# Kernel optimization log

Measured on AMD Instinct MI355X. Metric: run time of the kernel, lower is better.

The kernel has to match this reference:

```python
import jax, jax.numpy as jnp
import numpy as np

B, S, E, H = 2, 2048, 2048, 16
NOPE, ROPE, VD = 128, 64, 128
QH = NOPE + ROPE  # 192
LORA = 512
ROPE_THETA = 10000.0
EPS = 1e-6


def setup_inputs() -> dict:
    key = jax.random.key(0)
    ks = jax.random.split(key, 5)
    sd = lambda n: 1.0 / np.sqrt(n)
    return {
        "x": jax.random.normal(ks[0], (B, S, E), jnp.float32),
        "wq": jax.random.normal(ks[1], (E, H * QH), jnp.float32) * sd(E),
        "wkv_a": jax.random.normal(ks[2], (E, LORA + ROPE), jnp.float32) * sd(E),
        "wkv_b": jax.random.normal(ks[3], (LORA, H * (NOPE + VD)), jnp.float32) * sd(LORA),
        "wo": jax.random.normal(ks[4], (H * VD, E), jnp.float32) * sd(H * VD),
        "kv_norm_scale": jnp.ones((LORA,), jnp.float32),
    }


def _rope(xp, cos, sin):
    # xp: (..., s, d); cos/sin: (s, d//2)
    d2 = xp.shape[-1] // 2
    x1, x2 = xp[..., :d2], xp[..., d2:]
    return jnp.concatenate([x1 * cos - x2 * sin, x2 * cos + x1 * sin], axis=-1)


def reference(x, wq, wkv_a, wkv_b, wo, kv_norm_scale):
    b, s, _ = x.shape
    # queries: (b, H, s, QH), split into no-pe / pe slices
    q = (x @ wq).reshape(b, s, H, QH).transpose(0, 2, 1, 3)
    q_nope, q_pe = q[..., :NOPE], q[..., NOPE:]

    # low-rank KV latent projection
    kva = x @ wkv_a  # (b, s, LORA + ROPE)
    ckv, k_pe = kva[..., :LORA], kva[..., LORA:]
    ckv = ckv * jax.lax.rsqrt(jnp.mean(ckv * ckv, axis=-1, keepdims=True) + EPS)
    ckv = ckv * kv_norm_scale  # RMSNorm on latent
    kv = (ckv @ wkv_b).reshape(b, s, H, NOPE + VD).transpose(0, 2, 1, 3)
    k_nope, v = kv[..., :NOPE], kv[..., NOPE:]

    # partial RoPE on the rope slice only
    pos = jnp.arange(s, dtype=jnp.float32)
    inv = 1.0 / (ROPE_THETA ** (jnp.arange(0, ROPE, 2, dtype=jnp.float32) / ROPE))
    ang = pos[:, None] * inv  # (s, ROPE//2)
    cos, sin = jnp.cos(ang), jnp.sin(ang)
    q_pe = _rope(q_pe, cos, sin)                 # (b, H, s, ROPE)
    k_pe = _rope(k_pe[:, None, :, :], cos, sin)  # (b, 1, s, ROPE), shared over heads

    # concat (the new_empty + slice-write in torch)
    qs = jnp.concatenate([q_nope, q_pe], axis=-1)  # (b, H, s, QH)
    ks_ = jnp.concatenate(
        [k_nope, jnp.broadcast_to(k_pe, (b, H, s, ROPE))], axis=-1
    )  # (b, H, s, QH)

    # causal SDPA with scale = q_head_dim**-0.5; asymmetric V head dim
    scale = QH ** -0.5
    scores = jnp.einsum('bhqd,bhkd->bhqk', qs, ks_) * scale
    causal = jnp.tril(jnp.ones((s, s), dtype=bool))
    scores = jnp.where(causal, scores, jnp.finfo(scores.dtype).min)
    attn = jax.nn.softmax(scores, axis=-1)
    out = jnp.einsum('bhqk,bhkd->bhqd', attn, v)  # (b, H, s, VD)
    out = out.transpose(0, 2, 1, 3).reshape(b, s, H * VD)
    return out @ wo
```

## Files before the change

kernel.cpp:

```cpp
#include <hip/hip_runtime.h>
#include <stdint.h>
#include <stddef.h>

typedef __bf16 bf16x8 __attribute__((ext_vector_type(8)));
typedef float floatx4 __attribute__((ext_vector_type(4)));
typedef unsigned short u16;

__device__ __forceinline__ float bf2f(u16 h) {
    unsigned u = ((unsigned)h) << 16;
    return __builtin_bit_cast(float, u);
}
__device__ __forceinline__ u16 f2bf(float f) {
    unsigned u = __builtin_bit_cast(unsigned, f);
    u += 0x7fffu + ((u >> 16) & 1u);
    return (u16)(u >> 16);
}

__device__ __forceinline__ void gload16(const void* g, void* l) {
    __builtin_amdgcn_global_load_lds(
        (const __attribute__((address_space(1))) uint32_t*)g,
        (__attribute__((address_space(3))) uint32_t*)l, 16, 0, 0);
}

__device__ __forceinline__ void wait_vm8() { asm volatile("s_waitcnt vmcnt(8)" ::: "memory"); }
__device__ __forceinline__ void wait_vm6() { asm volatile("s_waitcnt vmcnt(6)" ::: "memory"); }
__device__ __forceinline__ void wait_vm4() { asm volatile("s_waitcnt vmcnt(4)" ::: "memory"); }
__device__ __forceinline__ void wait_vm3() { asm volatile("s_waitcnt vmcnt(3)" ::: "memory"); }
__device__ __forceinline__ void wait_vm0() { asm volatile("s_waitcnt vmcnt(0)" ::: "memory"); }

__global__ __launch_bounds__(256) void k_conv_x(const float* __restrict__ in,
                                                u16* __restrict__ out, int n8) {
    int i = blockIdx.x * 256 + threadIdx.x;
    if (i >= n8) return;
    const float* f = in + (size_t)i * 8;
    unsigned o[4];
    for (int t = 0; t < 4; t++) {
        u16 lo = f2bf(f[2 * t]), hi = f2bf(f[2 * t + 1]);
        o[t] = (unsigned)lo | ((unsigned)hi << 16);
    }
    uint4 p = {o[0], o[1], o[2], o[3]};
    *(uint4*)&out[(size_t)i * 8] = p;
}

__global__ __launch_bounds__(256) void k_convT(const float* __restrict__ in,
                                               u16* __restrict__ out, int K, int N) {
    __shared__ u16 t[32][33];
    int k0 = blockIdx.x * 32, n0 = blockIdx.y * 32;
    int c = threadIdx.x & 31, r8 = threadIdx.x >> 5;
    for (int j = 0; j < 4; j++) {
        int row = r8 + j * 8;
        int n = n0 + c;
        t[row][c] = (n < N) ? f2bf(in[(size_t)(k0 + row) * N + n]) : (u16)0;
    }
    __syncthreads();
    for (int j = 0; j < 4; j++) {
        int row = r8 + j * 8;
        out[(size_t)(n0 + row) * K + k0 + c] = t[c][row];
    }
}

__global__ __launch_bounds__(256) void k_transpose_v(const u16* __restrict__ kv,
                                                     u16* __restrict__ vt) {
    __shared__ u16 t[32][33];
    int bh = blockIdx.z;
    int s0 = blockIdx.x * 32, v0 = blockIdx.y * 32;
    int c = threadIdx.x & 31, r8 = threadIdx.x >> 5;
    int b = bh >> 4, h = bh & 15;
    for (int j = 0; j < 4; j++) {
        int s = s0 + r8 + j * 8;
        t[r8 + j * 8][c] = kv[(size_t)(b * 2048 + s) * 4096 + h * 256 + 128 + v0 + c];
    }
    __syncthreads();
    for (int j = 0; j < 4; j++) {
        int v = v0 + r8 + j * 8;
        vt[((size_t)bh * 128 + v) * 2048 + s0 + c] = t[c][r8 + j * 8];
    }
}

template <int NWC, int MODE>
__global__ __launch_bounds__(512, 2) void k_gemm256(const u16* __restrict__ A,
                                                    const u16* __restrict__ BT,
                                                    void* __restrict__ C0,
                                                    void* __restrict__ C1,
                                                    int K, int ldc) {
    constexpr int MFR = 16 / (8 / NWC);
    constexpr int ACH = 2;
    constexpr int BCH = NWC / 2;
    constexpr int SLOT = 8192 + NWC * 2048;
    __shared__ __align__(16) u16 RING[4][SLOT];
    int tid = threadIdx.x;
    int w = tid >> 6, lane = tid & 63;
    int l15 = lane & 15, quad = lane >> 4;
    int wr = w / NWC, wc = w % NWC;

    int gx = gridDim.x;
    int nwg = gx * gridDim.y;
    int flat = blockIdx.y * gx + blockIdx.x;
    int cpx = nwg >> 3;
    int swz = (flat & 7) * cpx + (flat >> 3);
    int bx = swz % gx, by = swz / gx;
    size_t m0 = (size_t)bx * 256, n0 = (size_t)by * (NWC * 64);
    int NT = K >> 5;

    const u16* srcA[ACH];
    const u16* srcB[BCH];
    int ldsAb[ACH], ldsBb[BCH];
#pragma unroll
    for (int p = 0; p < ACH; p++) {
        int chunk = p * 512 + tid;
        int s = chunk >> 6;
        int b = (chunk & 63) * 8;
        int bu = b ^ (((b >> 8) & 1) << 4);
        int r = bu >> 5, c = bu & 31;
        srcA[p] = A + (m0 + s * 16 + r) * (size_t)K + c;
        ldsAb[p] = (p * 512 + w * 64) * 8;
    }
#pragma unroll
    for (int p = 0; p < BCH; p++) {
        int chunk = p * 512 + tid;
        int s = chunk >> 6;
        int b = (chunk & 63) * 8;
        int bu = b ^ (((b >> 8) & 1) << 4);
        int r = bu >> 5, c = bu & 31;
        srcB[p] = BT + (n0 + s * 16 + r) * (size_t)K + c;
        ldsBb[p] = 8192 + (p * 512 + w * 64) * 8;
    }

    const int swb = (l15 * 32 + quad * 8) ^ ((l15 >> 3) << 4);

    floatx4 acc[MFR][4];
    const floatx4 fzero = {0.f, 0.f, 0.f, 0.f};
#pragma unroll
    for (int i = 0; i < MFR; i++)
#pragma unroll
        for (int j = 0; j < 4; j++) acc[i][j] = fzero;

    bf16x8 aA[MFR], bB[4];

    auto STAGE = [&](int j) {
        int rs = j & 3;
        size_t ko = (size_t)j * 32;
        u16* ring = &RING[rs][0];
#pragma unroll
        for (int p = 0; p < ACH; p++) gload16(srcA[p] + ko, ring + ldsAb[p]);
#pragma unroll
        for (int p = 0; p < BCH; p++) gload16(srcB[p] + ko, ring + ldsBb[p]);
    };
    auto READ = [&](int rs) {
        const u16* ring = &RING[rs][0];
#pragma unroll
        for (int i2 = 0; i2 < MFR; i2++)
            aA[i2] = *(const bf16x8*)&ring[(wr * MFR + i2) * 512 + swb];
#pragma unroll
        for (int j2 = 0; j2 < 4; j2++)
            bB[j2] = *(const bf16x8*)&ring[8192 + (wc * 4 + j2) * 512 + swb];
    };
    auto MMA = [&]() {
        __builtin_amdgcn_s_setprio(1);
#pragma unroll
        for (int i2 = 0; i2 < MFR; i2++)
#pragma unroll
            for (int j2 = 0; j2 < 4; j2++)
                acc[i2][j2] = __builtin_amdgcn_mfma_f32_16x16x32_bf16(
                    aA[i2], bB[j2], acc[i2][j2], 0, 0, 0);
        __builtin_amdgcn_s_setprio(0);
    };

    STAGE(0); STAGE(1); STAGE(2);

    int j = 0;
    for (; j + 3 < NT; j++) {
        if constexpr (NWC == 4) wait_vm8(); else wait_vm6();
        __builtin_amdgcn_s_barrier();
        __builtin_amdgcn_sched_barrier(0);
        READ(j & 3);
        STAGE(j + 3);
        __builtin_amdgcn_sched_barrier(0);
        MMA();
    }
    {
        if constexpr (NWC == 4) wait_vm8(); else wait_vm6();
        __builtin_amdgcn_s_barrier();
        __builtin_amdgcn_sched_barrier(0);
        READ(j & 3); MMA(); j++;
    }
    {
        if constexpr (NWC == 4) wait_vm4(); else wait_vm3();
        __builtin_amdgcn_s_barrier();
        __builtin_amdgcn_sched_barrier(0);
        READ(j & 3); MMA(); j++;
    }
    {
        wait_vm0();
        __builtin_amdgcn_s_barrier();
        __builtin_amdgcn_sched_barrier(0);
        READ(j & 3); MMA();
    }

#pragma unroll
    for (int i = 0; i < MFR; i++)
#pragma unroll
        for (int j2 = 0; j2 < 4; j2++) {
            size_t col = n0 + wc * 64 + j2 * 16 + l15;
#pragma unroll
            for (int r = 0; r < 4; r++) {
                size_t row = m0 + (size_t)wr * (MFR * 16) + i * 16 + quad * 4 + r;
                if constexpr (MODE == 0) {
                    ((u16*)C0)[row * ldc + col] = f2bf(acc[i][j2][r]);
                } else if constexpr (MODE == 1) {
                    ((float*)C0)[row * ldc + col] = acc[i][j2][r];
                } else {
                    if (col < 3072)
                        ((u16*)C0)[row * 3072 + col] = f2bf(acc[i][j2][r]);
                    else if (col < 3648)
                        ((u16*)C1)[row * 576 + (col - 3072)] = f2bf(acc[i][j2][r]);
                }
            }
        }
}

__global__ __launch_bounds__(64) void k_rmsnorm(const u16* __restrict__ kva,
                                                const float* __restrict__ scl,
                                                u16* __restrict__ ckv) {
    int r = blockIdx.x, lane = threadIdx.x;
    const u16* row = kva + (size_t)r * 576 + lane * 8;
    uint4 raw = *(const uint4*)row;
    unsigned w[4] = {raw.x, raw.y, raw.z, raw.w};
    float f[8];
    float ss = 0.f;
    for (int t = 0; t < 4; t++) {
        f[2 * t]     = bf2f((u16)(w[t] & 0xffffu));
        f[2 * t + 1] = bf2f((u16)(w[t] >> 16));
        ss += f[2 * t] * f[2 * t] + f[2 * t + 1] * f[2 * t + 1];
    }
    for (int off = 1; off < 64; off <<= 1) ss += __shfl_xor(ss, off, 64);
    float rs = rsqrtf(ss * (1.f / 512.f) + 1e-6f);
    unsigned o[4];
    for (int t = 0; t < 4; t++) {
        u16 lo = f2bf(f[2 * t] * rs * scl[lane * 8 + 2 * t]);
        u16 hi = f2bf(f[2 * t + 1] * rs * scl[lane * 8 + 2 * t + 1]);
        o[t] = (unsigned)lo | ((unsigned)hi << 16);
    }
    uint4 packed = {o[0], o[1], o[2], o[3]};
    *(uint4*)(ckv + (size_t)r * 512 + lane * 8) = packed;
}

__global__ __launch_bounds__(256) void k_rope(u16* __restrict__ qbuf, u16* __restrict__ kva) {
    int tid = threadIdx.x;
    int rloc = tid >> 7;
    int task = tid & 127;
    int r = blockIdx.x * 2 + rloc;
    __shared__ float cs_s[2][32], sn_s[2][32];
    if (tid < 64) {
        int rr = tid >> 5, i = tid & 31;
        int ss = (blockIdx.x * 2 + rr) & 2047;
        float freq = __expf(-0.28782313662425575f * (float)i);
        float ang = (float)ss * freq;
        float sn, cs;
        sincosf(ang, &sn, &cs);
        cs_s[rr][i] = cs; sn_s[rr][i] = sn;
    }
    __syncthreads();
    if (task < 68) {
        int rb = task >> 2, q = task & 3;
        u16* base = (rb < 16) ? qbuf + (size_t)r * 3072 + rb * 192 + 128
                              : kva + (size_t)r * 576 + 512;
        u16* p1 = base + q * 8;
        uint4 x1v = *(uint4*)p1;
        uint4 x2v = *(uint4*)(p1 + 32);
        unsigned w1[4] = {x1v.x, x1v.y, x1v.z, x1v.w};
        unsigned w2[4] = {x2v.x, x2v.y, x2v.z, x2v.w};
        unsigned o1[4], o2[4];
        for (int t2 = 0; t2 < 4; t2++) {
            float a1 = bf2f((u16)(w1[t2] & 0xffffu)), b1 = bf2f((u16)(w1[t2] >> 16));
            float a2 = bf2f((u16)(w2[t2] & 0xffffu)), b2 = bf2f((u16)(w2[t2] >> 16));
            int i0 = q * 8 + t2 * 2, i1 = i0 + 1;
            float c0 = cs_s[rloc][i0], s0 = sn_s[rloc][i0];
            float c1 = cs_s[rloc][i1], s1 = sn_s[rloc][i1];
            o1[t2] = (unsigned)f2bf(a1 * c0 - a2 * s0) | ((unsigned)f2bf(b1 * c1 - b2 * s1) << 16);
            o2[t2] = (unsigned)f2bf(a2 * c0 + a1 * s0) | ((unsigned)f2bf(b2 * c1 + b1 * s1) << 16);
        }
        uint4 y1 = {o1[0], o1[1], o1[2], o1[3]};
        uint4 y2 = {o2[0], o2[1], o2[2], o2[3]};
        *(uint4*)p1 = y1;
        *(uint4*)(p1 + 32) = y2;
    }
}

__global__ __launch_bounds__(256, 3) void k_attn(const u16* __restrict__ qbuf,
                                                 const u16* __restrict__ kv,
                                                 const u16* __restrict__ kva,
                                                 const u16* __restrict__ vt,
                                                 u16* __restrict__ attno) {
    int tid = threadIdx.x;
    int wave = tid >> 6, lane = tid & 63;
    int quad = lane >> 4, l15 = lane & 15;
    int hb = blockIdx.x;
    int h = hb & 15, b = hb >> 4;
    int qb = 31 - (int)blockIdx.y;
    int qg0 = qb * 64 + wave * 16;
    int row = qg0 + l15;

    __shared__ __align__(16) u16 Kn[2][32 * 136];
    __shared__ __align__(16) u16 Kp[2][32 * 72];
    __shared__ __align__(16) u16 Vs[2][128 * 40];
    __shared__ __align__(16) u16 P[4][16 * 40];

    const u16* qrp = qbuf + ((size_t)(b * 2048) + qg0 + l15) * 3072 + h * 192;
    bf16x8 qf[6];
    for (int c = 0; c < 6; c++) qf[c] = *(const bf16x8*)&qrp[c * 32 + quad * 8];

    const floatx4 fzero = {0.f, 0.f, 0.f, 0.f};
    floatx4 o[8];
    for (int f = 0; f < 8; f++) o[f] = fzero;
    float lp = 0.f;

    const u16* kvb = kv  + (size_t)(b * 2048) * 4096 + h * 256;
    const u16* kpb = kva + (size_t)(b * 2048) * 576 + 512;
    const u16* vtb = vt  + (size_t)(b * 16 + h) * 128 * 2048;
    const float scale = 0.07216878364870323f;

    int nkt = qb * 2 + 2;

    int kKey0 = tid >> 4,          kOff0 = (tid & 15) * 8;
    int kKey1 = (tid + 256) >> 4,  kOff1 = (tid & 15) * 8;
    int pKey  = tid >> 3,          pOff  = (tid & 7) * 8;
    int vRow0 = tid >> 2,          vOff0 = (tid & 3) * 8;
    int vRow1 = (tid + 256) >> 2,  vOff1 = (tid & 3) * 8;

    {
        uint4 a = *(const uint4*)&kvb[(size_t)kKey0 * 4096 + kOff0];
        uint4 c = *(const uint4*)&kvb[(size_t)kKey1 * 4096 + kOff1];
        uint4 d = *(const uint4*)&kpb[(size_t)pKey * 576 + pOff];
        uint4 e = *(const uint4*)&vtb[(size_t)vRow0 * 2048 + vOff0];
        uint4 g = *(const uint4*)&vtb[(size_t)vRow1 * 2048 + vOff1];
        *(uint4*)&Kn[0][kKey0 * 136 + kOff0] = a;
        *(uint4*)&Kn[0][kKey1 * 136 + kOff1] = c;
        *(uint4*)&Kp[0][pKey * 72 + pOff] = d;
        *(uint4*)&Vs[0][vRow0 * 40 + vOff0] = e;
        *(uint4*)&Vs[0][vRow1 * 40 + vOff1] = g;
    }
    __syncthreads();

    for (int kt = 0; kt < nkt; kt++) {
        int cur = kt & 1;
        bool have = (kt + 1) < nkt;
        uint4 sA = {}, sB = {}, sC = {}, sD = {}, sE = {};
        if (have) {
            int kb = (kt + 1) * 32;
            sA = *(const uint4*)&kvb[(size_t)(kb + kKey0) * 4096 + kOff0];
            sB = *(const uint4*)&kvb[(size_t)(kb + kKey1) * 4096 + kOff1];
            sC = *(const uint4*)&kpb[(size_t)(kb + pKey) * 576 + pOff];
            sD = *(const uint4*)&vtb[(size_t)vRow0 * 2048 + kb + vOff0];
            sE = *(const uint4*)&vtb[(size_t)vRow1 * 2048 + kb + vOff1];
        }
        if (kt * 32 <= qg0 + 15) {
            bf16x8 vf[8];
            for (int f = 0; f < 8; f++)
                vf[f] = *(const bf16x8*)&Vs[cur][(f * 16 + l15) * 40 + quad * 8];
            floatx4 sc[2] = {fzero, fzero};
            __builtin_amdgcn_s_setprio(1);
            for (int hf = 0; hf < 2; hf++) {
                const u16* kn = &Kn[cur][(hf * 16 + l15) * 136];
                const u16* kp = &Kp[cur][(hf * 16 + l15) * 72];
                for (int c = 0; c < 4; c++) {
                    bf16x8 kf = *(const bf16x8*)&kn[c * 32 + quad * 8];
                    sc[hf] = __builtin_amdgcn_mfma_f32_16x16x32_bf16(kf, qf[c], sc[hf], 0, 0, 0);
                }
                for (int c = 0; c < 2; c++) {
                    bf16x8 kf = *(const bf16x8*)&kp[c * 32 + quad * 8];
                    sc[hf] = __builtin_amdgcn_mfma_f32_16x16x32_bf16(kf, qf[4 + c], sc[hf], 0, 0, 0);
                }
            }
            __builtin_amdgcn_s_setprio(0);
            asm volatile("" ::: "memory");
            for (int hf = 0; hf < 2; hf++) {
                int keyb = kt * 32 + hf * 16 + quad * 4;
                float p[4];
                for (int r = 0; r < 4; r++)
                    p[r] = (keyb + r <= row) ? __expf(sc[hf][r] * scale) : 0.f;
                lp += (p[0] + p[1]) + (p[2] + p[3]);
                unsigned d0 = (unsigned)f2bf(p[0]) | ((unsigned)f2bf(p[1]) << 16);
                unsigned d1 = (unsigned)f2bf(p[2]) | ((unsigned)f2bf(p[3]) << 16);
                uint2 pk = {d0, d1};
                *(uint2*)&P[wave][l15 * 40 + hf * 16 + quad * 4] = pk;
            }
            asm volatile("" ::: "memory");
            bf16x8 pa = *(const bf16x8*)&P[wave][l15 * 40 + quad * 8];
            asm volatile("" ::: "memory");
            __builtin_amdgcn_s_setprio(1);
            for (int f = 0; f < 8; f++)
                o[f] = __builtin_amdgcn_mfma_f32_16x16x32_bf16(pa, vf[f], o[f], 0, 0, 0);
            __builtin_amdgcn_s_setprio(0);
        }
        if (have) {
            int nb = cur ^ 1;
            *(uint4*)&Kn[nb][kKey0 * 136 + kOff0] = sA;
            *(uint4*)&Kn[nb][kKey1 * 136 + kOff1] = sB;
            *(uint4*)&Kp[nb][pKey * 72 + pOff] = sC;
            *(uint4*)&Vs[nb][vRow0 * 40 + vOff0] = sD;
            *(uint4*)&Vs[nb][vRow1 * 40 + vOff1] = sE;
        }
        __syncthreads();
    }

    lp += __shfl_xor(lp, 16, 64);
    lp += __shfl_xor(lp, 32, 64);
    float lrow[4];
    for (int r = 0; r < 4; r++) lrow[r] = __shfl(lp, quad * 4 + r, 64);
    for (int f = 0; f < 8; f++)
        for (int r = 0; r < 4; r++) {
            int orow = qg0 + quad * 4 + r;
            float val = o[f][r] / lrow[r];
            attno[((size_t)(b * 2048) + orow) * 2048 + h * 128 + f * 16 + l15] = f2bf(val);
        }
}

extern "C" void kernel_launch(void* const* d_in, const int* in_sizes, int n_in,
                              void* d_out, int out_size, void* d_ws, size_t ws_size,
                              hipStream_t stream) {
    const float* x_raw    = (const float*)d_in[0];
    const float* wq_raw   = (const float*)d_in[1];
    const float* wkva_raw = (const float*)d_in[2];
    const float* wkvb_raw = (const float*)d_in[3];
    const float* wo_raw   = (const float*)d_in[4];
    const float* kvs_raw  = (const float*)d_in[5];
    float* out = (float*)d_out;
    u16* ws = (u16*)d_ws;

    const size_t O_ATT = 0;
    const size_t O_VT  = 8388608;
    const size_t O_QB  = 16777216;
    const size_t O_KVA = 29360128;
    const size_t O_KV  = 31719424;
    const size_t TOTAL_BYTES = 48496640ull * 2;
    if (ws_size < TOTAL_BYTES) return;

    u16* g12bt  = ws + O_ATT;
    u16* ckv    = ws + O_ATT;
    u16* wkvb_t = ws + O_ATT + 2097152;
    u16* attno  = ws + O_ATT;
    u16* x_bf   = ws + O_VT;
    u16* vt     = ws + O_VT;
    u16* qbuf   = ws + O_QB;
    u16* wo_t   = ws + O_QB;
    u16* kva    = ws + O_KVA;
    u16* kv     = ws + O_KV;

    k_conv_x<<<4096, 256, 0, stream>>>(x_raw, x_bf, 1048576);
    k_convT<<<dim3(64, 96), 256, 0, stream>>>(wq_raw, g12bt, 2048, 3072);
    k_convT<<<dim3(64, 20), 256, 0, stream>>>(wkva_raw, g12bt + (size_t)3072 * 2048, 2048, 576);

    k_gemm256<2, 2><<<dim3(16, 29), 512, 0, stream>>>(x_bf, g12bt, qbuf, kva, 2048, 0);

    k_rmsnorm<<<4096, 64, 0, stream>>>(kva, kvs_raw, ckv);
    k_convT<<<dim3(16, 128), 256, 0, stream>>>(wkvb_raw, wkvb_t, 512, 4096);
    k_gemm256<4, 0><<<dim3(16, 16), 512, 0, stream>>>(ckv, wkvb_t, kv, nullptr, 512, 4096);

    k_rope<<<2048, 256, 0, stream>>>(qbuf, kva);
    k_transpose_v<<<dim3(64, 4, 32), 256, 0, stream>>>(kv, vt);

    k_attn<<<dim3(32, 32), 256, 0, stream>>>(qbuf, kv, kva, vt, attno);

    k_convT<<<dim3(64, 64), 256, 0, stream>>>(wo_raw, wo_t, 2048, 2048);
    k_gemm256<2, 1><<<dim3(16, 16), 512, 0, stream>>>(attno, wo_t, out, nullptr, 2048, 2048);
}
```

Measured before the change: 397.0 us.

## Fuse V transpose into kv GEMM epilogue and double-buffer GEMM fragment reads

Removes the separate V transpose kernel: the kv_b GEMM now runs in a new epilogue mode that writes K-nope rows normally and stores V transposed directly into the vt buffer. It also switches that GEMM to the 2-column-wave tile config with more blocks. The GEMM main loop is restructured to ping-pong register fragments across two K-steps so LDS reads overlap MFMAs, and setprio hints are removed from the GEMM and attention MMAs. The transposed V stores are strided 8-byte writes, which may be poorly coalesced.

```diff
diff --git a/kernel.cpp b/kernel.cpp
--- a/kernel.cpp
+++ b/kernel.cpp
@@ -56,24 +56,6 @@
     for (int j = 0; j < 4; j++) {
         int row = r8 + j * 8;
         out[(size_t)(n0 + row) * K + k0 + c] = t[c][row];
-    }
-}
-
-__global__ __launch_bounds__(256) void k_transpose_v(const u16* __restrict__ kv,
-                                                     u16* __restrict__ vt) {
-    __shared__ u16 t[32][33];
-    int bh = blockIdx.z;
-    int s0 = blockIdx.x * 32, v0 = blockIdx.y * 32;
-    int c = threadIdx.x & 31, r8 = threadIdx.x >> 5;
-    int b = bh >> 4, h = bh & 15;
-    for (int j = 0; j < 4; j++) {
-        int s = s0 + r8 + j * 8;
-        t[r8 + j * 8][c] = kv[(size_t)(b * 2048 + s) * 4096 + h * 256 + 128 + v0 + c];
-    }
-    __syncthreads();
-    for (int j = 0; j < 4; j++) {
-        int v = v0 + r8 + j * 8;
-        vt[((size_t)bh * 128 + v) * 2048 + s0 + c] = t[c][r8 + j * 8];
     }
 }
 
@@ -135,7 +117,7 @@
 #pragma unroll
         for (int j = 0; j < 4; j++) acc[i][j] = fzero;
 
-    bf16x8 aA[MFR], bB[4];
+    bf16x8 aA0[MFR], bB0[4], aA1[MFR], bB1[4];
 
     auto STAGE = [&](int j) {
         int rs = j & 3;
@@ -146,55 +128,64 @@
 #pragma unroll
         for (int p = 0; p < BCH; p++) gload16(srcB[p] + ko, ring + ldsBb[p]);
     };
-    auto READ = [&](int rs) {
+    auto READ0 = [&](int rs) {
         const u16* ring = &RING[rs][0];
 #pragma unroll
         for (int i2 = 0; i2 < MFR; i2++)
-            aA[i2] = *(const bf16x8*)&ring[(wr * MFR + i2) * 512 + swb];
+            aA0[i2] = *(const bf16x8*)&ring[(wr * MFR + i2) * 512 + swb];
 #pragma unroll
         for (int j2 = 0; j2 < 4; j2++)
-            bB[j2] = *(const bf16x8*)&ring[8192 + (wc * 4 + j2) * 512 + swb];
+            bB0[j2] = *(const bf16x8*)&ring[8192 + (wc * 4 + j2) * 512 + swb];
     };
-    auto MMA = [&]() {
-        __builtin_amdgcn_s_setprio(1);
+    auto READ1 = [&](int rs) {
+        const u16* ring = &RING[rs][0];
+#pragma unroll
+        for (int i2 = 0; i2 < MFR; i2++)
+            aA1[i2] = *(const bf16x8*)&ring[(wr * MFR + i2) * 512 + swb];
+#pragma unroll
+        for (int j2 = 0; j2 < 4; j2++)
+            bB1[j2] = *(const bf16x8*)&ring[8192 + (wc * 4 + j2) * 512 + swb];
+    };
+    auto MMA0 = [&]() {
 #pragma unroll
         for (int i2 = 0; i2 < MFR; i2++)
 #pragma unroll
             for (int j2 = 0; j2 < 4; j2++)
                 acc[i2][j2] = __builtin_amdgcn_mfma_f32_16x16x32_bf16(
-                    aA[i2], bB[j2], acc[i2][j2], 0, 0, 0);
-        __builtin_amdgcn_s_setprio(0);
+                    aA0[i2], bB0[j2], acc[i2][j2], 0, 0, 0);
     };
+    auto MMA1 = [&]() {
+#pragma unroll
+        for (int i2 = 0; i2 < MFR; i2++)
+#pragma unroll
+            for (int j2 = 0; j2 < 4; j2++)
+                acc[i2][j2] = __builtin_amdgcn_mfma_f32_16x16x32_bf16(
+                    aA1[i2], bB1[j2], acc[i2][j2], 0, 0, 0);
+    };
 
     STAGE(0); STAGE(1); STAGE(2);
-
-    int j = 0;
-    for (; j + 3 < NT; j++) {
-        if constexpr (NWC == 4) wait_vm8(); else wait_vm6();
+    if constexpr (NWC == 4) wait_vm8(); else wait_vm6();
+    __builtin_amdgcn_s_barrier();
+    __builtin_amdgcn_sched_barrier(0);
+    READ0(0);
+
+    for (int j = 0; j + 1 < NT; j += 2) {
+        if (j + 2 < NT) { if constexpr (NWC == 4) wait_vm4(); else wait_vm3(); }
+        else wait_vm0();
         __builtin_amdgcn_s_barrier();
         __builtin_amdgcn_sched_barrier(0);
-        READ(j & 3);
-        STAGE(j + 3);
-        __builtin_amdgcn_sched_barrier(0);
-        MMA();
-    }
-    {
-        if constexpr (NWC == 4) wait_vm8(); else wait_vm6();
-        __builtin_amdgcn_s_barrier();
-        __builtin_amdgcn_sched_barrier(0);
-        READ(j & 3); MMA(); j++;
-    }
-    {
-        if constexpr (NWC == 4) wait_vm4(); else wait_vm3();
-        __builtin_amdgcn_s_barrier();
-        __builtin_amdgcn_sched_barrier(0);
-        READ(j & 3); MMA(); j++;
-    }
-    {
-        wait_vm0();
-        __builtin_amdgcn_s_barrier();
-        __builtin_amdgcn_sched_barrier(0);
-        READ(j & 3); MMA();
+        READ1((j + 1) & 3);
+        if (j + 3 < NT) STAGE(j + 3);
+        MMA0();
+        if (j + 2 < NT) {
+            if (j + 3 < NT) { if constexpr (NWC == 4) wait_vm4(); else wait_vm3(); }
+            else wait_vm0();
+            __builtin_amdgcn_s_barrier();
+            __builtin_amdgcn_sched_barrier(0);
+            READ0((j + 2) & 3);
+            if (j + 4 < NT) STAGE(j + 4);
+        }
+        MMA1();
     }
 
 #pragma unroll
@@ -209,11 +200,27 @@
                     ((u16*)C0)[row * ldc + col] = f2bf(acc[i][j2][r]);
                 } else if constexpr (MODE == 1) {
                     ((float*)C0)[row * ldc + col] = acc[i][j2][r];
-                } else {
+                } else if constexpr (MODE == 2) {
                     if (col < 3072)
                         ((u16*)C0)[row * 3072 + col] = f2bf(acc[i][j2][r]);
                     else if (col < 3648)
                         ((u16*)C1)[row * 576 + (col - 3072)] = f2bf(acc[i][j2][r]);
+                }
+            }
+            if constexpr (MODE == 3) {
+                int cm = (int)(col & 255);
+                size_t row0 = m0 + (size_t)wr * (MFR * 16) + i * 16 + quad * 4;
+                if (cm < 128) {
+#pragma unroll
+                    for (int r = 0; r < 4; r++)
+                        ((u16*)C0)[(row0 + r) * 4096 + col] = f2bf(acc[i][j2][r]);
+                } else {
+                    int h = (int)(col >> 8), vd = cm - 128;
+                    size_t b = row0 >> 11, s = row0 & 2047;
+                    unsigned lo = (unsigned)f2bf(acc[i][j2][0]) | ((unsigned)f2bf(acc[i][j2][1]) << 16);
+                    unsigned hi = (unsigned)f2bf(acc[i][j2][2]) | ((unsigned)f2bf(acc[i][j2][3]) << 16);
+                    uint2 pk = {lo, hi};
+                    *(uint2*)&((u16*)C1)[(((b << 4) + h) * 128 + vd) * 2048 + s] = pk;
                 }
             }
         }
@@ -359,7 +366,6 @@
             for (int f = 0; f < 8; f++)
                 vf[f] = *(const bf16x8*)&Vs[cur][(f * 16 + l15) * 40 + quad * 8];
             floatx4 sc[2] = {fzero, fzero};
-            __builtin_amdgcn_s_setprio(1);
             for (int hf = 0; hf < 2; hf++) {
                 const u16* kn = &Kn[cur][(hf * 16 + l15) * 136];
                 const u16* kp = &Kp[cur][(hf * 16 + l15) * 72];
@@ -372,7 +378,6 @@
                     sc[hf] = __builtin_amdgcn_mfma_f32_16x16x32_bf16(kf, qf[4 + c], sc[hf], 0, 0, 0);
                 }
             }
-            __builtin_amdgcn_s_setprio(0);
             asm volatile("" ::: "memory");
             for (int hf = 0; hf < 2; hf++) {
                 int keyb = kt * 32 + hf * 16 + quad * 4;
@@ -388,10 +393,8 @@
             asm volatile("" ::: "memory");
             bf16x8 pa = *(const bf16x8*)&P[wave][l15 * 40 + quad * 8];
             asm volatile("" ::: "memory");
-            __builtin_amdgcn_s_setprio(1);
             for (int f = 0; f < 8; f++)
                 o[f] = __builtin_amdgcn_mfma_f32_16x16x32_bf16(pa, vf[f], o[f], 0, 0, 0);
-            __builtin_amdgcn_s_setprio(0);
         }
         if (have) {
             int nb = cur ^ 1;
@@ -455,10 +458,9 @@
 
     k_rmsnorm<<<4096, 64, 0, stream>>>(kva, kvs_raw, ckv);
     k_convT<<<dim3(16, 128), 256, 0, stream>>>(wkvb_raw, wkvb_t, 512, 4096);
-    k_gemm256<4, 0><<<dim3(16, 16), 512, 0, stream>>>(ckv, wkvb_t, kv, nullptr, 512, 4096);
+    k_gemm256<2, 3><<<dim3(16, 32), 512, 0, stream>>>(ckv, wkvb_t, kv, vt, 512, 4096);
 
     k_rope<<<2048, 256, 0, stream>>>(qbuf, kva);
-    k_transpose_v<<<dim3(64, 4, 32), 256, 0, stream>>>(kv, vt);
 
     k_attn<<<dim3(32, 32), 256, 0, stream>>>(qbuf, kv, kva, vt, attno);
 
```

New measurement: 372.6 us. -6.1%, faster.
